# Kernel optimization log

Measured on AMD Instinct MI355X. Metric: run time of the kernel, lower is better.

Reference implementation:

```python
import jax, jax.numpy as jnp
import numpy as np

Q, N = 8, 256          # number of sub-networks, state dim per network
QN = Q * N             # 2048 total state dimension
BS = 128               # batch size
TMAX = 128             # time steps
STEP = 0.01            # Euler integration step size


def _offdiag_block_mask(q, n):
    # L_mask: ones everywhere except the q diagonal n x n blocks
    diag_blocks = np.kron(np.eye(q), np.ones((n, n)))
    return jnp.asarray(1.0 - diag_blocks, dtype=jnp.float32)


def setup_inputs() -> dict:
    key = jax.random.key(0)
    ks = jax.random.split(key, 6)
    s = 1.0 / np.sqrt(QN)  # keep 128-step Euler recurrence numerically tame
    X0 = jax.random.normal(ks[0], (BS, QN), dtype=jnp.float32)
    A = jax.random.normal(ks[1], (QN, QN), dtype=jnp.float32) * s
    B = jax.random.normal(ks[2], (QN, QN), dtype=jnp.float32) * s
    W = jax.random.normal(ks[3], (QN, QN), dtype=jnp.float32) * s
    # P is block-diagonal and well-conditioned (I + small block-diag noise)
    blk = np.kron(np.eye(Q), np.ones((N, N))).astype(np.float32)
    P = jnp.eye(QN, dtype=jnp.float32) + 0.1 * jax.random.normal(ks[4], (QN, QN), dtype=jnp.float32) * jnp.asarray(blk)
    bx = jax.random.normal(ks[5], (QN,), dtype=jnp.float32)
    return {"X0": X0, "A": A, "B": B, "W": W, "P": P, "bx": bx, "tmax": TMAX}


def reference(X0, A, B, W, P, bx, tmax):
    # mask GL weight to off-block-diagonal coupling, then L = W - P^{-1} W^T P
    Wm = W * _offdiag_block_mask(Q, N)
    L = Wm - jnp.linalg.solve(P, Wm.T @ P)
    M = A + L                      # (qn, qn)
    Xi0 = X0.T                     # (qn, bs)
    b = bx[:, None]                # (qn, 1) broadcast over batch

    def step_fn(Xi, _):
        Xn = Xi + STEP * (M @ Xi + B @ jax.nn.relu(Xi) + b)
        return Xn, Xn

    _, Xs = jax.lax.scan(step_fn, Xi0, None, length=tmax - 1)  # (tmax-1, qn, bs)
    X = jnp.concatenate([Xi0[None], Xs], axis=0)               # (tmax, qn, bs)
    return jnp.transpose(X, (2, 0, 1))                          # (bs, tmax, qn)
```

## Files before the change

### kernel.cpp

```cpp
#include <hip/hip_runtime.h>

typedef unsigned short u16;
typedef __attribute__((ext_vector_type(8))) short bf16x8;
typedef __attribute__((ext_vector_type(4))) float f32x4;
typedef __attribute__((ext_vector_type(4))) unsigned short u16x4;

#define QN    2048
#define BSZ   128
#define TMAXK 128
#define STEPF 0.01f
#define NEWTON_ITERS 46

__device__ __forceinline__ u16 f2bf(float f){
  unsigned u = __float_as_uint(f);
  u += 0x7fffu + ((u >> 16) & 1u);
  return (u16)(u >> 16);
}
__device__ __forceinline__ float bf2f(u16 h){
  return __uint_as_float(((unsigned)h) << 16);
}


__global__ __launch_bounds__(256) void alpha_k(const float* __restrict__ P, float* __restrict__ alpha){
  int q = blockIdx.x, i = threadIdx.x;
  const float* Pb = P + (size_t)(q << 8) * QN + (q << 8);
  float rs = 0.f, cs = 0.f;
  for (int c = 0; c < 256; ++c){
    rs += fabsf(Pb[(size_t)i * QN + c]);
    cs += fabsf(Pb[(size_t)c * QN + i]);
  }
  __shared__ float red[256];
  red[i] = rs; __syncthreads();
  for (int o = 128; o > 0; o >>= 1){ if (i < o) red[i] = fmaxf(red[i], red[i+o]); __syncthreads(); }
  float mr = red[0];
  __syncthreads();
  red[i] = cs; __syncthreads();
  for (int o = 128; o > 0; o >>= 1){ if (i < o) red[i] = fmaxf(red[i], red[i+o]); __syncthreads(); }
  if (i == 0) alpha[q] = mr * red[0];
}

__global__ __launch_bounds__(256) void initV_k(const float* __restrict__ P, const float* __restrict__ alpha, float* __restrict__ V){
  int idx = blockIdx.x * 256 + threadIdx.x;
  int q = idx >> 16, rc = idx & 65535;
  int r = rc >> 8, c = rc & 255;
  V[idx] = P[(size_t)((q << 8) + c) * QN + (q << 8) + r] / alpha[q];
}

__global__ __launch_bounds__(256) void newton_T_k(const float* __restrict__ P, const float* __restrict__ Vin, float* __restrict__ Tm){
  int q = blockIdx.x >> 4;
  int tl = blockIdx.x & 15;
  int rb = (tl >> 2) << 6, cb = (tl & 3) << 6;
  const float* Ab = P + (size_t)(q << 8) * QN + (q << 8);
  const float* Bb = Vin + (q << 16);
  __shared__ float Asm[16][68];
  __shared__ float Bsm[16][68];
  int tid = threadIdx.x, ty = tid >> 4, tx = tid & 15;
  float acc[4][4];
#pragma unroll
  for (int i = 0; i < 4; i++)
#pragma unroll
    for (int j = 0; j < 4; j++) acc[i][j] = 0.f;
  int ar = tid >> 2, ak = (tid & 3) << 2;
  int bc = tid & 63, bk = tid >> 6;
  for (int kb = 0; kb < 256; kb += 16){
    f32x4 av = *(const f32x4*)(Ab + (size_t)(rb + ar) * QN + kb + ak);
    float b0 = Bb[(size_t)(kb + bk     ) * 256 + cb + bc];
    float b1 = Bb[(size_t)(kb + bk +  4) * 256 + cb + bc];
    float b2 = Bb[(size_t)(kb + bk +  8) * 256 + cb + bc];
    float b3 = Bb[(size_t)(kb + bk + 12) * 256 + cb + bc];
    __syncthreads();
    Asm[ak+0][ar] = av.x; Asm[ak+1][ar] = av.y; Asm[ak+2][ar] = av.z; Asm[ak+3][ar] = av.w;
    Bsm[bk   ][bc] = b0;  Bsm[bk+ 4][bc] = b1;  Bsm[bk+ 8][bc] = b2;  Bsm[bk+12][bc] = b3;
    __syncthreads();
#pragma unroll
    for (int kk = 0; kk < 16; kk++){
      f32x4 a = *(const f32x4*)&Asm[kk][ty << 2];
      f32x4 b = *(const f32x4*)&Bsm[kk][tx << 2];
#pragma unroll
      for (int i = 0; i < 4; i++)
#pragma unroll
        for (int j = 0; j < 4; j++) acc[i][j] += a[i] * b[j];
    }
  }
  float* Ob = Tm + (q << 16);
#pragma unroll
  for (int i = 0; i < 4; i++){
    f32x4 o; o.x = acc[i][0]; o.y = acc[i][1]; o.z = acc[i][2]; o.w = acc[i][3];
    *(f32x4*)(Ob + (size_t)(rb + (ty << 2) + i) * 256 + cb + (tx << 2)) = o;
  }
}

__global__ __launch_bounds__(256) void newton_V_k(const float* __restrict__ Vin, const float* __restrict__ Tm, float* __restrict__ Vout){
  int q = blockIdx.x >> 4;
  int tl = blockIdx.x & 15;
  int rb = (tl >> 2) << 6, cb = (tl & 3) << 6;
  const float* Ab = Vin + (q << 16);
  const float* Bb = Tm + (q << 16);
  __shared__ float Asm[16][68];
  __shared__ float Bsm[16][68];
  int tid = threadIdx.x, ty = tid >> 4, tx = tid & 15;
  float acc[4][4];
#pragma unroll
  for (int i = 0; i < 4; i++)
#pragma unroll
    for (int j = 0; j < 4; j++) acc[i][j] = 0.f;
  int ar = tid >> 2, ak = (tid & 3) << 2;
  int bc = tid & 63, bk = tid >> 6;
  for (int kb = 0; kb < 256; kb += 16){
    f32x4 av = *(const f32x4*)(Ab + (size_t)(rb + ar) * 256 + kb + ak);
    float b0 = Bb[(size_t)(kb + bk     ) * 256 + cb + bc];
    float b1 = Bb[(size_t)(kb + bk +  4) * 256 + cb + bc];
    float b2 = Bb[(size_t)(kb + bk +  8) * 256 + cb + bc];
    float b3 = Bb[(size_t)(kb + bk + 12) * 256 + cb + bc];
    __syncthreads();
    Asm[ak+0][ar] = av.x; Asm[ak+1][ar] = av.y; Asm[ak+2][ar] = av.z; Asm[ak+3][ar] = av.w;
    Bsm[bk   ][bc] = b0;  Bsm[bk+ 4][bc] = b1;  Bsm[bk+ 8][bc] = b2;  Bsm[bk+12][bc] = b3;
    __syncthreads();
#pragma unroll
    for (int kk = 0; kk < 16; kk++){
      f32x4 a = *(const f32x4*)&Asm[kk][ty << 2];
      f32x4 b = *(const f32x4*)&Bsm[kk][tx << 2];
#pragma unroll
      for (int i = 0; i < 4; i++)
#pragma unroll
        for (int j = 0; j < 4; j++) acc[i][j] += a[i] * b[j];
    }
  }
  float* Ob = Vout + (q << 16);
#pragma unroll
  for (int i = 0; i < 4; i++){
    f32x4 vo = *(const f32x4*)(Ab + (size_t)(rb + (ty << 2) + i) * 256 + cb + (tx << 2));
    f32x4 o;
    o.x = 2.f*vo.x - acc[i][0]; o.y = 2.f*vo.y - acc[i][1];
    o.z = 2.f*vo.z - acc[i][2]; o.w = 2.f*vo.w - acc[i][3];
    *(f32x4*)(Ob + (size_t)(rb + (ty << 2) + i) * 256 + cb + (tx << 2)) = o;
  }
}

__global__ __launch_bounds__(256) void build_Y_k(const float* __restrict__ W, const float* __restrict__ P, float* __restrict__ Ymat){
  int j  = blockIdx.x >> 7;
  int rt = (blockIdx.x >> 2) & 31;
  int ct = blockIdx.x & 3;
  int rb = rt << 6, cb = ct << 6, jb = j << 8;
  int tid = threadIdx.x, ty = tid >> 4, tx = tid & 15;
  if ((rt >> 2) == j){
#pragma unroll
    for (int i = 0; i < 4; i++){
      f32x4 z = {0.f, 0.f, 0.f, 0.f};
      *(f32x4*)(Ymat + (size_t)(rb + (ty << 2) + i) * QN + jb + cb + (tx << 2)) = z;
    }
    return;
  }
  __shared__ float Asm[16][68];
  __shared__ float Bsm[16][68];
  float acc[4][4];
#pragma unroll
  for (int i = 0; i < 4; i++)
#pragma unroll
    for (int j2 = 0; j2 < 4; j2++) acc[i][j2] = 0.f;
  int sr = tid & 63, sk = tid >> 6;
  for (int kb = 0; kb < 256; kb += 16){
    float a0 = W[(size_t)(jb + kb + sk     ) * QN + rb + sr];
    float a1 = W[(size_t)(jb + kb + sk +  4) * QN + rb + sr];
    float a2 = W[(size_t)(jb + kb + sk +  8) * QN + rb + sr];
    float a3 = W[(size_t)(jb + kb + sk + 12) * QN + rb + sr];
    float b0 = P[(size_t)(jb + kb + sk     ) * QN + jb + cb + sr];
    float b1 = P[(size_t)(jb + kb + sk +  4) * QN + jb + cb + sr];
    float b2 = P[(size_t)(jb + kb + sk +  8) * QN + jb + cb + sr];
    float b3 = P[(size_t)(jb + kb + sk + 12) * QN + jb + cb + sr];
    __syncthreads();
    Asm[sk   ][sr] = a0; Asm[sk+ 4][sr] = a1; Asm[sk+ 8][sr] = a2; Asm[sk+12][sr] = a3;
    Bsm[sk   ][sr] = b0; Bsm[sk+ 4][sr] = b1; Bsm[sk+ 8][sr] = b2; Bsm[sk+12][sr] = b3;
    __syncthreads();
#pragma unroll
    for (int kk = 0; kk < 16; kk++){
      f32x4 a = *(const f32x4*)&Asm[kk][ty << 2];
      f32x4 b = *(const f32x4*)&Bsm[kk][tx << 2];
#pragma unroll
      for (int i = 0; i < 4; i++)
#pragma unroll
        for (int j2 = 0; j2 < 4; j2++) acc[i][j2] += a[i] * b[j2];
    }
  }
#pragma unroll
  for (int i = 0; i < 4; i++){
    f32x4 o; o.x = acc[i][0]; o.y = acc[i][1]; o.z = acc[i][2]; o.w = acc[i][3];
    *(f32x4*)(Ymat + (size_t)(rb + (ty << 2) + i) * QN + jb + cb + (tx << 2)) = o;
  }
}

__global__ __launch_bounds__(256) void build_C_k(const float* __restrict__ Vfin, const float* __restrict__ Ymat,
                                                 const float* __restrict__ Ain, const float* __restrict__ W,
                                                 u16* __restrict__ C1, u16* __restrict__ C2){
  int ib = blockIdx.x >> 7;
  int rest = blockIdx.x & 127;
  int rt = rest >> 5, ct = rest & 31;
  int rb = rt << 6, cb = ct << 6;
  const float* Ab = Vfin + (ib << 16);
  __shared__ float Asm[16][68];
  __shared__ float Bsm[16][68];
  int tid = threadIdx.x, ty = tid >> 4, tx = tid & 15;
  float acc[4][4];
#pragma unroll
  for (int i = 0; i < 4; i++)
#pragma unroll
    for (int j = 0; j < 4; j++) acc[i][j] = 0.f;
  int ar = tid >> 2, ak = (tid & 3) << 2;
  int bc = tid & 63, bk = tid >> 6;
  for (int kb = 0; kb < 256; kb += 16){
    f32x4 av = *(const f32x4*)(Ab + (size_t)(rb + ar) * 256 + kb + ak);
    float b0 = Ymat[(size_t)((ib << 8) + kb + bk     ) * QN + cb + bc];
    float b1 = Ymat[(size_t)((ib << 8) + kb + bk +  4) * QN + cb + bc];
    float b2 = Ymat[(size_t)((ib << 8) + kb + bk +  8) * QN + cb + bc];
    float b3 = Ymat[(size_t)((ib << 8) + kb + bk + 12) * QN + cb + bc];
    __syncthreads();
    Asm[ak+0][ar] = av.x; Asm[ak+1][ar] = av.y; Asm[ak+2][ar] = av.z; Asm[ak+3][ar] = av.w;
    Bsm[bk   ][bc] = b0;  Bsm[bk+ 4][bc] = b1;  Bsm[bk+ 8][bc] = b2;  Bsm[bk+12][bc] = b3;
    __syncthreads();
#pragma unroll
    for (int kk = 0; kk < 16; kk++){
      f32x4 a = *(const f32x4*)&Asm[kk][ty << 2];
      f32x4 b = *(const f32x4*)&Bsm[kk][tx << 2];
#pragma unroll
      for (int i = 0; i < 4; i++)
#pragma unroll
        for (int j = 0; j < 4; j++) acc[i][j] += a[i] * b[j];
    }
  }
#pragma unroll
  for (int i = 0; i < 4; i++){
    int row = (ib << 8) + rb + (ty << 2) + i;
#pragma unroll
    for (int j = 0; j < 4; j++){
      int col = cb + (tx << 2) + j;
      float wv = ((row >> 8) == (col >> 8)) ? 0.f : W[(size_t)row * QN + col];
      float m = Ain[(size_t)row * QN + col] + wv - acc[i][j];
      u16 hi = f2bf(m);
      u16 lo = f2bf(m - bf2f(hi));
      C1[((size_t)row << 12) + col] = hi;
      C2[((size_t)row << 12) + col] = lo;
    }
  }
}

__global__ __launch_bounds__(256) void split_B_k(const float* __restrict__ Bin, u16* __restrict__ C1, u16* __restrict__ C2){
  int idx = blockIdx.x * 256 + threadIdx.x;
  int r = idx >> 11, c = idx & 2047;
  float v = Bin[idx];
  u16 hi = f2bf(v);
  u16 lo = f2bf(v - bf2f(hi));
  C1[((size_t)r << 12) + 2048 + c] = hi;
  C2[((size_t)r << 12) + 2048 + c] = lo;
}

__global__ __launch_bounds__(256) void init_state_k(const float* __restrict__ X0, float* __restrict__ Xf,
                                                    u16* __restrict__ Yst, float* __restrict__ out){
  int idx = blockIdx.x * 256 + threadIdx.x;
  int bs = idx >> 11, qn = idx & 2047;
  float x = X0[idx];
  Xf[idx] = x;
  Yst[((size_t)bs << 12) + qn] = f2bf(x);
  Yst[((size_t)bs << 12) + 2048 + qn] = f2bf(fmaxf(x, 0.f));
  out[((size_t)bs * TMAXK) * QN + qn] = x;
}


__global__ __launch_bounds__(256) void step_gemm_k(const u16* __restrict__ C1, const u16* __restrict__ C2,
                                                   const u16* __restrict__ Yst, float* __restrict__ part){
  __shared__ __align__(16) char lds[65536];
  int tid = threadIdx.x;
  int b = blockIdx.x;
  int s = b & 7, rg = b >> 3;
  int k0 = s << 9;
  for (int it = 0; it < 16; ++it){
    int e = it * 256 + tid;
    const u16* src = (e < 2048) ? C1 : C2;
    int el = e & 2047;
    int r = el >> 6;
    int k8 = (el & 63) << 3;
    bf16x8 v = *(const bf16x8*)(src + ((size_t)((rg << 5) + r) << 12) + k0 + k8);
    int addr = ((e >> 11) << 15) + (((r << 10) + (k8 << 1)) ^ ((r & 7) << 4));
    *(bf16x8*)(lds + addr) = v;
  }
  __syncthreads();
  int w = tid >> 6, l = tid & 63;
  int lo16 = l & 15, hi = l >> 4;
  f32x4 acc[2][2];
#pragma unroll
  for (int m = 0; m < 2; m++)
#pragma unroll
    for (int n = 0; n < 2; n++) acc[m][n] = (f32x4){0.f, 0.f, 0.f, 0.f};
  const u16* yb = Yst + ((size_t)((w << 5) + lo16) << 12) + k0 + (hi << 3);
#pragma unroll
  for (int kt = 0; kt < 16; ++kt){
    bf16x8 b0 = *(const bf16x8*)(yb + (kt << 5));
    bf16x8 b1 = *(const bf16x8*)(yb + (16 << 12) + (kt << 5));
    int kb2 = ((kt << 5) + (hi << 3)) << 1;
#pragma unroll
    for (int m = 0; m < 2; m++){
      int row = (m << 4) + lo16;
      int ba = ((row << 10) + kb2) ^ ((row & 7) << 4);
      bf16x8 a1 = *(const bf16x8*)(lds + ba);
      bf16x8 a2 = *(const bf16x8*)(lds + 32768 + ba);
      acc[m][0] = __builtin_amdgcn_mfma_f32_16x16x32_bf16(a1, b0, acc[m][0], 0, 0, 0);
      acc[m][0] = __builtin_amdgcn_mfma_f32_16x16x32_bf16(a2, b0, acc[m][0], 0, 0, 0);
      acc[m][1] = __builtin_amdgcn_mfma_f32_16x16x32_bf16(a1, b1, acc[m][1], 0, 0, 0);
      acc[m][1] = __builtin_amdgcn_mfma_f32_16x16x32_bf16(a2, b1, acc[m][1], 0, 0, 0);
    }
  }
#pragma unroll
  for (int m = 0; m < 2; m++)
#pragma unroll
    for (int n = 0; n < 2; n++){
      int bs = (w << 5) + (n << 4) + lo16;
      int row = (rg << 5) + (m << 4) + (hi << 2);
      __builtin_nontemporal_store(acc[m][n], (f32x4*)(part + ((size_t)((s << 7) + bs) << 11) + row));
    }
}

__global__ __launch_bounds__(256) void step_update_k(const float* __restrict__ part, float* __restrict__ Xf,
                                                     const float* __restrict__ bx, u16* __restrict__ Yst,
                                                     float* __restrict__ out, int t){
  int tid = blockIdx.x * 256 + threadIdx.x;
  int bs = tid >> 9;
  int row = (tid & 511) << 2;
  size_t base = ((size_t)bs << 11) + row;
  f32x4 u = {0.f, 0.f, 0.f, 0.f};
#pragma unroll
  for (int s = 0; s < 8; s++){
    f32x4 p = __builtin_nontemporal_load((const f32x4*)(part + ((size_t)((s << 7) + bs) << 11) + row));
    u += p;
  }
  f32x4 x = *(const f32x4*)(Xf + base);
  f32x4 b = *(const f32x4*)(bx + row);
  f32x4 xn = x + STEPF * (u + b);
  *(f32x4*)(Xf + base) = xn;
  __builtin_nontemporal_store(xn, (f32x4*)(out + ((size_t)((bs << 7) + t) << 11) + row));
  u16x4 hv, rv;
  hv.x = f2bf(xn.x); hv.y = f2bf(xn.y); hv.z = f2bf(xn.z); hv.w = f2bf(xn.w);
  rv.x = f2bf(fmaxf(xn.x, 0.f)); rv.y = f2bf(fmaxf(xn.y, 0.f));
  rv.z = f2bf(fmaxf(xn.z, 0.f)); rv.w = f2bf(fmaxf(xn.w, 0.f));
  *(u16x4*)(Yst + ((size_t)bs << 12) + row) = hv;
  *(u16x4*)(Yst + ((size_t)bs << 12) + 2048 + row) = rv;
}


extern "C" void kernel_launch(void* const* d_in, const int* in_sizes, int n_in,
                              void* d_out, int out_size, void* d_ws, size_t ws_size,
                              hipStream_t stream){
  (void)in_sizes; (void)n_in; (void)out_size; (void)ws_size;
  const float* X0  = (const float*)d_in[0];
  const float* Ain = (const float*)d_in[1];
  const float* Bin = (const float*)d_in[2];
  const float* Win = (const float*)d_in[3];
  const float* Pin = (const float*)d_in[4];
  const float* bx  = (const float*)d_in[5];
  float* out = (float*)d_out;
  char* ws = (char*)d_ws;
  const size_t MB = 1u << 20;

  u16*   C1    = (u16*)(ws);
  u16*   C2    = (u16*)(ws + 16*MB);
  float* Xf    = (float*)(ws + 32*MB);
  u16*   Yst   = (u16*)(ws + 33*MB);
  float* Ymat  = (float*)(ws + 34*MB);
  float* part  = (float*)(ws + 34*MB);
  float* Vb0   = (float*)(ws + 50*MB);
  float* Vb1   = (float*)(ws + 52*MB);
  float* Tm    = (float*)(ws + 54*MB);
  float* alpha = (float*)(ws + 56*MB);

  alpha_k<<<8, 256, 0, stream>>>(Pin, alpha);
  initV_k<<<2048, 256, 0, stream>>>(Pin, alpha, Vb0);
  float* Vc = Vb0; float* Vo = Vb1;
  for (int it = 0; it < NEWTON_ITERS; ++it){
    newton_T_k<<<128, 256, 0, stream>>>(Pin, Vc, Tm);
    newton_V_k<<<128, 256, 0, stream>>>(Vc, Tm, Vo);
    float* tmp = Vc; Vc = Vo; Vo = tmp;
  }
  build_Y_k<<<1024, 256, 0, stream>>>(Win, Pin, Ymat);
  build_C_k<<<1024, 256, 0, stream>>>(Vc, Ymat, Ain, Win, C1, C2);
  split_B_k<<<16384, 256, 0, stream>>>(Bin, C1, C2);
  init_state_k<<<1024, 256, 0, stream>>>(X0, Xf, Yst, out);

  for (int t = 1; t < TMAXK; ++t){
    step_gemm_k<<<512, 256, 0, stream>>>(C1, C2, Yst, part);
    step_update_k<<<256, 256, 0, stream>>>(part, Xf, bx, Yst, out, t);
  }
}
```

Before: 3.486 ms.

## Fuse per-step GEMM and state update via last-block atomic counter reduction

Merges the per-step GEMM and update kernels into one launch. The last of the 8 split-K blocks for each row group, found through an atomic counter, reduces the partial sums and writes the new state. The retiling stages the state operand (Yst) in LDS and streams the C1/C2 weights straight from global memory, using 512-thread blocks and 128KB of dynamic shared memory. Double-buffered Yst avoids read/write races across row groups. This cuts the launch count in half but serializes the reduction onto a few blocks and depends on threadfence ordering.

```diff
diff --git a/kernel.cpp b/kernel.cpp
--- a/kernel.cpp
+++ b/kernel.cpp
@@ -265,83 +265,80 @@
 }
 
 
-__global__ __launch_bounds__(256) void step_gemm_k(const u16* __restrict__ C1, const u16* __restrict__ C2,
-                                                   const u16* __restrict__ Yst, float* __restrict__ part){
-  __shared__ __align__(16) char lds[65536];
-  int tid = threadIdx.x;
-  int b = blockIdx.x;
+__global__ void __launch_bounds__(512, 1) step_k(
+    const u16* __restrict__ C1, const u16* __restrict__ C2,
+    const u16* __restrict__ YstR, u16* __restrict__ YstW,
+    float* __restrict__ part, float* __restrict__ Xf,
+    const float* __restrict__ bx, float* __restrict__ out,
+    unsigned* __restrict__ cnt, int t){
+  extern __shared__ char lds[];
+  int b = blockIdx.x, tid = threadIdx.x;
   int s = b & 7, rg = b >> 3;
-  int k0 = s << 9;
+  int k0 = s << 9, R = rg << 6;
   for (int it = 0; it < 16; ++it){
-    int e = it * 256 + tid;
-    const u16* src = (e < 2048) ? C1 : C2;
-    int el = e & 2047;
-    int r = el >> 6;
-    int k8 = (el & 63) << 3;
-    bf16x8 v = *(const bf16x8*)(src + ((size_t)((rg << 5) + r) << 12) + k0 + k8);
-    int addr = ((e >> 11) << 15) + (((r << 10) + (k8 << 1)) ^ ((r & 7) << 4));
+    int e = it * 512 + tid;
+    int bs = e >> 6;
+    int k8 = (e & 63) << 3;
+    bf16x8 v = *(const bf16x8*)(YstR + ((size_t)bs << 12) + k0 + k8);
+    int addr = (bs << 10) + ((k8 << 1) ^ ((bs & 7) << 4));
     *(bf16x8*)(lds + addr) = v;
   }
   __syncthreads();
   int w = tid >> 6, l = tid & 63;
   int lo16 = l & 15, hi = l >> 4;
-  f32x4 acc[2][2];
-#pragma unroll
-  for (int m = 0; m < 2; m++)
-#pragma unroll
-    for (int n = 0; n < 2; n++) acc[m][n] = (f32x4){0.f, 0.f, 0.f, 0.f};
-  const u16* yb = Yst + ((size_t)((w << 5) + lo16) << 12) + k0 + (hi << 3);
-#pragma unroll
+  int g = w >> 1, h = w & 1;
+  int row16 = R + (g << 4) + lo16;
+  const u16* a1p = C1 + ((size_t)row16 << 12) + k0 + (hi << 3);
+  const u16* a2p = C2 + ((size_t)row16 << 12) + k0 + (hi << 3);
+  f32x4 acc[4];
+#pragma unroll
+  for (int n = 0; n < 4; n++) acc[n] = (f32x4){0.f, 0.f, 0.f, 0.f};
+#pragma unroll 4
   for (int kt = 0; kt < 16; ++kt){
-    bf16x8 b0 = *(const bf16x8*)(yb + (kt << 5));
-    bf16x8 b1 = *(const bf16x8*)(yb + (16 << 12) + (kt << 5));
-    int kb2 = ((kt << 5) + (hi << 3)) << 1;
-#pragma unroll
-    for (int m = 0; m < 2; m++){
-      int row = (m << 4) + lo16;
-      int ba = ((row << 10) + kb2) ^ ((row & 7) << 4);
-      bf16x8 a1 = *(const bf16x8*)(lds + ba);
-      bf16x8 a2 = *(const bf16x8*)(lds + 32768 + ba);
-      acc[m][0] = __builtin_amdgcn_mfma_f32_16x16x32_bf16(a1, b0, acc[m][0], 0, 0, 0);
-      acc[m][0] = __builtin_amdgcn_mfma_f32_16x16x32_bf16(a2, b0, acc[m][0], 0, 0, 0);
-      acc[m][1] = __builtin_amdgcn_mfma_f32_16x16x32_bf16(a1, b1, acc[m][1], 0, 0, 0);
-      acc[m][1] = __builtin_amdgcn_mfma_f32_16x16x32_bf16(a2, b1, acc[m][1], 0, 0, 0);
-    }
-  }
-#pragma unroll
-  for (int m = 0; m < 2; m++)
-#pragma unroll
-    for (int n = 0; n < 2; n++){
-      int bs = (w << 5) + (n << 4) + lo16;
-      int row = (rg << 5) + (m << 4) + (hi << 2);
-      __builtin_nontemporal_store(acc[m][n], (f32x4*)(part + ((size_t)((s << 7) + bs) << 11) + row));
-    }
-}
-
-__global__ __launch_bounds__(256) void step_update_k(const float* __restrict__ part, float* __restrict__ Xf,
-                                                     const float* __restrict__ bx, u16* __restrict__ Yst,
-                                                     float* __restrict__ out, int t){
-  int tid = blockIdx.x * 256 + threadIdx.x;
-  int bs = tid >> 9;
-  int row = (tid & 511) << 2;
-  size_t base = ((size_t)bs << 11) + row;
-  f32x4 u = {0.f, 0.f, 0.f, 0.f};
-#pragma unroll
-  for (int s = 0; s < 8; s++){
-    f32x4 p = __builtin_nontemporal_load((const f32x4*)(part + ((size_t)((s << 7) + bs) << 11) + row));
-    u += p;
-  }
-  f32x4 x = *(const f32x4*)(Xf + base);
-  f32x4 b = *(const f32x4*)(bx + row);
-  f32x4 xn = x + STEPF * (u + b);
-  *(f32x4*)(Xf + base) = xn;
-  __builtin_nontemporal_store(xn, (f32x4*)(out + ((size_t)((bs << 7) + t) << 11) + row));
-  u16x4 hv, rv;
-  hv.x = f2bf(xn.x); hv.y = f2bf(xn.y); hv.z = f2bf(xn.z); hv.w = f2bf(xn.w);
-  rv.x = f2bf(fmaxf(xn.x, 0.f)); rv.y = f2bf(fmaxf(xn.y, 0.f));
-  rv.z = f2bf(fmaxf(xn.z, 0.f)); rv.w = f2bf(fmaxf(xn.w, 0.f));
-  *(u16x4*)(Yst + ((size_t)bs << 12) + row) = hv;
-  *(u16x4*)(Yst + ((size_t)bs << 12) + 2048 + row) = rv;
+    bf16x8 a1 = *(const bf16x8*)(a1p + (kt << 5));
+    bf16x8 a2 = *(const bf16x8*)(a2p + (kt << 5));
+    int kbyte = ((hi << 3) + (kt << 5)) << 1;
+#pragma unroll
+    for (int n = 0; n < 4; ++n){
+      int bs = (h << 6) + (n << 4) + lo16;
+      bf16x8 bf = *(const bf16x8*)(lds + (bs << 10) + (kbyte ^ ((bs & 7) << 4)));
+      acc[n] = __builtin_amdgcn_mfma_f32_16x16x32_bf16(a1, bf, acc[n], 0, 0, 0);
+      acc[n] = __builtin_amdgcn_mfma_f32_16x16x32_bf16(a2, bf, acc[n], 0, 0, 0);
+    }
+  }
+#pragma unroll
+  for (int n = 0; n < 4; ++n){
+    int bs = (h << 6) + (n << 4) + lo16;
+    int row = R + (g << 4) + (hi << 2);
+    __builtin_nontemporal_store(acc[n], (f32x4*)(part + ((size_t)((s << 7) + bs) << 11) + row));
+  }
+  __syncthreads();
+  __shared__ unsigned lastFlag;
+  if (tid == 0){
+    __threadfence();
+    unsigned old = atomicAdd(cnt + rg, 1u);
+    lastFlag = (old == (unsigned)(8 * t - 1));
+  }
+  __syncthreads();
+  if (!lastFlag) return;
+  __threadfence();
+  int row = R + (tid & 63);
+  int bs0 = (tid >> 6) << 4;
+  float xb = bx[row];
+#pragma unroll
+  for (int j = 0; j < 16; ++j){
+    int bs = bs0 + j;
+    float u = 0.f;
+#pragma unroll
+    for (int ss = 0; ss < 8; ++ss)
+      u += __builtin_nontemporal_load(part + ((size_t)((ss << 7) + bs) << 11) + row);
+    size_t xo = ((size_t)bs << 11) + row;
+    float x = Xf[xo] + STEPF * (u + xb);
+    Xf[xo] = x;
+    __builtin_nontemporal_store(x, out + ((size_t)((bs << 7) + t) << 11) + row);
+    YstW[((size_t)bs << 12) + row] = f2bf(x);
+    YstW[((size_t)bs << 12) + 2048 + row] = f2bf(fmaxf(x, 0.f));
+  }
 }
 
 
@@ -362,9 +359,11 @@
   u16*   C1    = (u16*)(ws);
   u16*   C2    = (u16*)(ws + 16*MB);
   float* Xf    = (float*)(ws + 32*MB);
-  u16*   Yst   = (u16*)(ws + 33*MB);
+  u16*   Yst0  = (u16*)(ws + 33*MB);
   float* Ymat  = (float*)(ws + 34*MB);
   float* part  = (float*)(ws + 34*MB);
+  u16*   Yst1  = (u16*)(ws + 42*MB);
+  unsigned* cnt = (unsigned*)(ws + 43*MB);
   float* Vb0   = (float*)(ws + 50*MB);
   float* Vb1   = (float*)(ws + 52*MB);
   float* Tm    = (float*)(ws + 54*MB);
@@ -381,10 +380,13 @@
   build_Y_k<<<1024, 256, 0, stream>>>(Win, Pin, Ymat);
   build_C_k<<<1024, 256, 0, stream>>>(Vc, Ymat, Ain, Win, C1, C2);
   split_B_k<<<16384, 256, 0, stream>>>(Bin, C1, C2);
-  init_state_k<<<1024, 256, 0, stream>>>(X0, Xf, Yst, out);
-
+  init_state_k<<<1024, 256, 0, stream>>>(X0, Xf, Yst0, out);
+  hipMemsetAsync(cnt, 0, 32 * sizeof(unsigned), stream);
+
+  hipFuncSetAttribute((const void*)step_k, hipFuncAttributeMaxDynamicSharedMemorySize, 131072);
   for (int t = 1; t < TMAXK; ++t){
-    step_gemm_k<<<512, 256, 0, stream>>>(C1, C2, Yst, part);
-    step_update_k<<<256, 256, 0, stream>>>(part, Xf, bx, Yst, out, t);
-  }
-}
+    const u16* YstR = (t & 1) ? Yst0 : Yst1;
+    u16*       YstW = (t & 1) ? Yst1 : Yst0;
+    step_k<<<256, 512, 131072, stream>>>(C1, C2, YstR, YstW, part, Xf, bx, out, cnt, t);
+  }
+}
```

Measured after the change: 7.698 ms. 2.21x slower.

## Fuse Newton T/V kernels and DMA step GEMM tiles directly into LDS

Applied to the files above, without the earlier changes.

Merges the two Newton-Schulz GEMM kernels into one kernel per column strip. Each block computes a 256x16 strip of T=P*V into LDS and immediately forms 2V - V*T, so the Tm round-trip and half the launches per iteration go away. The step GEMM now loads its C1/C2 tiles with global_load_lds, writing straight into shared memory without passing through registers. To keep the existing LDS bank swizzle, the swizzle is pre-applied to the column layout of C1/C2 when they are built. The fused Newton kernel recomputes P*V for each strip, so more P traffic and FLOPs per block fall on 128 blocks.

```diff
diff --git a/kernel.cpp b/kernel.cpp
--- a/kernel.cpp
+++ b/kernel.cpp
@@ -10,6 +10,10 @@
 #define TMAXK 128
 #define STEPF 0.01f
 #define NEWTON_ITERS 46
+
+#define GLOAD_LDS16(gsrc, ldst) \
+  __builtin_amdgcn_global_load_lds((const __attribute__((address_space(1))) void*)(gsrc), \
+                                   (__attribute__((address_space(3))) void*)(ldst), 16, 0, 0)
 
 __device__ __forceinline__ u16 f2bf(float f){
   unsigned u = __float_as_uint(f);
@@ -46,31 +50,41 @@
   V[idx] = P[(size_t)((q << 8) + c) * QN + (q << 8) + r] / alpha[q];
 }
 
-__global__ __launch_bounds__(256) void newton_T_k(const float* __restrict__ P, const float* __restrict__ Vin, float* __restrict__ Tm){
-  int q = blockIdx.x >> 4;
-  int tl = blockIdx.x & 15;
-  int rb = (tl >> 2) << 6, cb = (tl & 3) << 6;
-  const float* Ab = P + (size_t)(q << 8) * QN + (q << 8);
-  const float* Bb = Vin + (q << 16);
-  __shared__ float Asm[16][68];
-  __shared__ float Bsm[16][68];
-  int tid = threadIdx.x, ty = tid >> 4, tx = tid & 15;
+__global__ __launch_bounds__(256) void newton_TV_k(const float* __restrict__ P,
+                                                   const float* __restrict__ Vin,
+                                                   float* __restrict__ Vout){
+  int q = blockIdx.x >> 4, st = blockIdx.x & 15;
+  int cb = st << 4;
+  const float* Pb = P + (size_t)(q << 8) * QN + (q << 8);
+  const float* Vb = Vin + (q << 16);
+  __shared__ float Asm[16][256];
+  __shared__ float Bsm[16][16];
+  __shared__ float Tb[256][16];
+  int tid = threadIdx.x, ty = tid >> 2, tx = tid & 3;
   float acc[4][4];
+
 #pragma unroll
   for (int i = 0; i < 4; i++)
 #pragma unroll
     for (int j = 0; j < 4; j++) acc[i][j] = 0.f;
-  int ar = tid >> 2, ak = (tid & 3) << 2;
-  int bc = tid & 63, bk = tid >> 6;
   for (int kb = 0; kb < 256; kb += 16){
-    f32x4 av = *(const f32x4*)(Ab + (size_t)(rb + ar) * QN + kb + ak);
-    float b0 = Bb[(size_t)(kb + bk     ) * 256 + cb + bc];
-    float b1 = Bb[(size_t)(kb + bk +  4) * 256 + cb + bc];
-    float b2 = Bb[(size_t)(kb + bk +  8) * 256 + cb + bc];
-    float b3 = Bb[(size_t)(kb + bk + 12) * 256 + cb + bc];
-    __syncthreads();
-    Asm[ak+0][ar] = av.x; Asm[ak+1][ar] = av.y; Asm[ak+2][ar] = av.z; Asm[ak+3][ar] = av.w;
-    Bsm[bk   ][bc] = b0;  Bsm[bk+ 4][bc] = b1;  Bsm[bk+ 8][bc] = b2;  Bsm[bk+12][bc] = b3;
+    f32x4 av[4];
+#pragma unroll
+    for (int rd = 0; rd < 4; ++rd){
+      int idx = rd * 256 + tid;
+      int row = idx >> 2, kq = (idx & 3) << 2;
+      av[rd] = *(const f32x4*)(Pb + (size_t)row * QN + kb + kq);
+    }
+    float bv = Vb[(size_t)(kb + (tid >> 4)) * 256 + cb + (tid & 15)];
+    __syncthreads();
+#pragma unroll
+    for (int rd = 0; rd < 4; ++rd){
+      int idx = rd * 256 + tid;
+      int row = idx >> 2, kq = (idx & 3) << 2;
+#pragma unroll
+      for (int u = 0; u < 4; ++u) Asm[kq + u][row] = av[rd][u];
+    }
+    Bsm[tid >> 4][tid & 15] = bv;
     __syncthreads();
 #pragma unroll
     for (int kk = 0; kk < 16; kk++){
@@ -82,44 +96,37 @@
         for (int j = 0; j < 4; j++) acc[i][j] += a[i] * b[j];
     }
   }
-  float* Ob = Tm + (q << 16);
 #pragma unroll
   for (int i = 0; i < 4; i++){
     f32x4 o; o.x = acc[i][0]; o.y = acc[i][1]; o.z = acc[i][2]; o.w = acc[i][3];
-    *(f32x4*)(Ob + (size_t)(rb + (ty << 2) + i) * 256 + cb + (tx << 2)) = o;
-  }
-}
-
-__global__ __launch_bounds__(256) void newton_V_k(const float* __restrict__ Vin, const float* __restrict__ Tm, float* __restrict__ Vout){
-  int q = blockIdx.x >> 4;
-  int tl = blockIdx.x & 15;
-  int rb = (tl >> 2) << 6, cb = (tl & 3) << 6;
-  const float* Ab = Vin + (q << 16);
-  const float* Bb = Tm + (q << 16);
-  __shared__ float Asm[16][68];
-  __shared__ float Bsm[16][68];
-  int tid = threadIdx.x, ty = tid >> 4, tx = tid & 15;
-  float acc[4][4];
+    *(f32x4*)&Tb[(ty << 2) + i][tx << 2] = o;
+  }
+
 #pragma unroll
   for (int i = 0; i < 4; i++)
 #pragma unroll
     for (int j = 0; j < 4; j++) acc[i][j] = 0.f;
-  int ar = tid >> 2, ak = (tid & 3) << 2;
-  int bc = tid & 63, bk = tid >> 6;
   for (int kb = 0; kb < 256; kb += 16){
-    f32x4 av = *(const f32x4*)(Ab + (size_t)(rb + ar) * 256 + kb + ak);
-    float b0 = Bb[(size_t)(kb + bk     ) * 256 + cb + bc];
-    float b1 = Bb[(size_t)(kb + bk +  4) * 256 + cb + bc];
-    float b2 = Bb[(size_t)(kb + bk +  8) * 256 + cb + bc];
-    float b3 = Bb[(size_t)(kb + bk + 12) * 256 + cb + bc];
-    __syncthreads();
-    Asm[ak+0][ar] = av.x; Asm[ak+1][ar] = av.y; Asm[ak+2][ar] = av.z; Asm[ak+3][ar] = av.w;
-    Bsm[bk   ][bc] = b0;  Bsm[bk+ 4][bc] = b1;  Bsm[bk+ 8][bc] = b2;  Bsm[bk+12][bc] = b3;
+    f32x4 av[4];
+#pragma unroll
+    for (int rd = 0; rd < 4; ++rd){
+      int idx = rd * 256 + tid;
+      int row = idx >> 2, kq = (idx & 3) << 2;
+      av[rd] = *(const f32x4*)(Vb + (size_t)row * 256 + kb + kq);
+    }
+    __syncthreads();
+#pragma unroll
+    for (int rd = 0; rd < 4; ++rd){
+      int idx = rd * 256 + tid;
+      int row = idx >> 2, kq = (idx & 3) << 2;
+#pragma unroll
+      for (int u = 0; u < 4; ++u) Asm[kq + u][row] = av[rd][u];
+    }
     __syncthreads();
 #pragma unroll
     for (int kk = 0; kk < 16; kk++){
       f32x4 a = *(const f32x4*)&Asm[kk][ty << 2];
-      f32x4 b = *(const f32x4*)&Bsm[kk][tx << 2];
+      f32x4 b = *(const f32x4*)&Tb[kb + kk][tx << 2];
 #pragma unroll
       for (int i = 0; i < 4; i++)
 #pragma unroll
@@ -129,11 +136,12 @@
   float* Ob = Vout + (q << 16);
 #pragma unroll
   for (int i = 0; i < 4; i++){
-    f32x4 vo = *(const f32x4*)(Ab + (size_t)(rb + (ty << 2) + i) * 256 + cb + (tx << 2));
+    int row = (ty << 2) + i;
+    f32x4 vo = *(const f32x4*)(Vb + (size_t)row * 256 + cb + (tx << 2));
     f32x4 o;
     o.x = 2.f*vo.x - acc[i][0]; o.y = 2.f*vo.y - acc[i][1];
     o.z = 2.f*vo.z - acc[i][2]; o.w = 2.f*vo.w - acc[i][3];
-    *(f32x4*)(Ob + (size_t)(rb + (ty << 2) + i) * 256 + cb + (tx << 2)) = o;
+    *(f32x4*)(Ob + (size_t)row * 256 + cb + (tx << 2)) = o;
   }
 }
 
@@ -230,6 +238,7 @@
 #pragma unroll
   for (int i = 0; i < 4; i++){
     int row = (ib << 8) + rb + (ty << 2) + i;
+    int sw = (row & 7) << 3;
 #pragma unroll
     for (int j = 0; j < 4; j++){
       int col = cb + (tx << 2) + j;
@@ -237,8 +246,9 @@
       float m = Ain[(size_t)row * QN + col] + wv - acc[i][j];
       u16 hi = f2bf(m);
       u16 lo = f2bf(m - bf2f(hi));
-      C1[((size_t)row << 12) + col] = hi;
-      C2[((size_t)row << 12) + col] = lo;
+      int colw = col ^ sw;
+      C1[((size_t)row << 12) + colw] = hi;
+      C2[((size_t)row << 12) + colw] = lo;
     }
   }
 }
@@ -249,8 +259,9 @@
   float v = Bin[idx];
   u16 hi = f2bf(v);
   u16 lo = f2bf(v - bf2f(hi));
-  C1[((size_t)r << 12) + 2048 + c] = hi;
-  C2[((size_t)r << 12) + 2048 + c] = lo;
+  int colw = (2048 + c) ^ ((r & 7) << 3);
+  C1[((size_t)r << 12) + colw] = hi;
+  C2[((size_t)r << 12) + colw] = lo;
 }
 
 __global__ __launch_bounds__(256) void init_state_k(const float* __restrict__ X0, float* __restrict__ Xf,
@@ -272,18 +283,15 @@
   int b = blockIdx.x;
   int s = b & 7, rg = b >> 3;
   int k0 = s << 9;
+  int w = tid >> 6, l = tid & 63;
+#pragma unroll
   for (int it = 0; it < 16; ++it){
-    int e = it * 256 + tid;
-    const u16* src = (e < 2048) ? C1 : C2;
-    int el = e & 2047;
-    int r = el >> 6;
-    int k8 = (el & 63) << 3;
-    bf16x8 v = *(const bf16x8*)(src + ((size_t)((rg << 5) + r) << 12) + k0 + k8);
-    int addr = ((e >> 11) << 15) + (((r << 10) + (k8 << 1)) ^ ((r & 7) << 4));
-    *(bf16x8*)(lds + addr) = v;
+    int c = it * 4 + w;
+    int p = c >> 5, r = c & 31;
+    const u16* src = (p == 0 ? C1 : C2) + ((size_t)((rg << 5) + r) << 12) + k0 + (l << 3);
+    GLOAD_LDS16(src, lds + c * 1024);
   }
   __syncthreads();
-  int w = tid >> 6, l = tid & 63;
   int lo16 = l & 15, hi = l >> 4;
   f32x4 acc[2][2];
 #pragma unroll
@@ -367,15 +375,13 @@
   float* part  = (float*)(ws + 34*MB);
   float* Vb0   = (float*)(ws + 50*MB);
   float* Vb1   = (float*)(ws + 52*MB);
-  float* Tm    = (float*)(ws + 54*MB);
   float* alpha = (float*)(ws + 56*MB);
 
   alpha_k<<<8, 256, 0, stream>>>(Pin, alpha);
   initV_k<<<2048, 256, 0, stream>>>(Pin, alpha, Vb0);
   float* Vc = Vb0; float* Vo = Vb1;
   for (int it = 0; it < NEWTON_ITERS; ++it){
-    newton_T_k<<<128, 256, 0, stream>>>(Pin, Vc, Tm);
-    newton_V_k<<<128, 256, 0, stream>>>(Vc, Tm, Vo);
+    newton_TV_k<<<128, 256, 0, stream>>>(Pin, Vc, Vo);
     float* tmp = Vc; Vc = Vo; Vo = tmp;
   }
   build_Y_k<<<1024, 256, 0, stream>>>(Win, Pin, Ymat);
```

Measured after the change: 3.709 ms. 6.4% more time.
